# Performance work log

Hardware: AMD Instinct MI355X
Metric: run time of the kernel (lower is better)

Reference implementation:

```python
import jax, jax.numpy as jnp
import numpy as np

N = 50000      # nodes
E = 800000     # edges (avg degree 16)
C = 16         # hidden states per generative model
M = 32         # discrete symbol alphabet size
G = 8          # n_gen


def setup_inputs() -> dict:
    key = jax.random.key(0)
    k = jax.random.split(key, 6)
    u = lambda kk, shp: jax.random.uniform(kk, shp, jnp.float32, -5.0, 5.0)
    return {
        "x": jax.random.randint(k[0], (N,), 0, M),
        "edge_index": jax.random.randint(k[1], (2, E), 0, N),
        "B0": u(k[2], (C, M, G)),       # CGMMLayer_0.B
        "Pi": u(k[3], (C, G)),          # CGMMLayer_0.Pi
        "B1": u(k[4], (C, M, G)),       # CGMMLayer.B
        "Q_neigh": u(k[5], (C, C, G)),  # CGMMLayer.Q_neigh
    }


def reference(x, edge_index, B0, Pi, B1, Q_neigh):
    n = x.shape[0]
    # ---- layer 0 (CGMMLayer_0) ----
    sm_B0 = jax.nn.softmax(B0, axis=1)   # [C,M,G], softmax over symbols
    sm_Pi = jax.nn.softmax(Pi, axis=0)   # [C,G],   softmax over states
    # unnorm_posterior = Pi * B[:, x]    -> [N,C,G]
    unnorm0 = sm_Pi[None, :, :] * jnp.transpose(sm_B0[:, x, :], (1, 0, 2))
    norm0 = unnorm0.sum(1, keepdims=True)           # [N,1,G]
    ll0 = jnp.log(norm0[:, 0, :])                   # [N,G]
    post0 = unnorm0 / norm0                         # [N,C,G] = h_prev
    # ---- layer 1 (CGMMLayer) ----
    sm_Q = jax.nn.softmax(Q_neigh, axis=0)          # [C,C,G], softmax over dim 0
    sm_B1 = jax.nn.softmax(B1, axis=1)              # [C,M,G]
    src, dst = edge_index[0], edge_index[1]
    gathered = post0[dst]                           # [E,C,G] edge gather
    aggr_sum = jax.ops.segment_sum(gathered, src, num_segments=n)   # [N,C,G]
    cnt = jax.ops.segment_sum(jnp.ones((src.shape[0],), jnp.float32), src, num_segments=n)
    aggr = aggr_sum / jnp.maximum(cnt, 1.0)[:, None, None]          # scatter-mean
    B_nodes = jnp.transpose(sm_B1[:, x, :], (1, 0, 2))[:, :, None, :]  # [N,C,1,G]
    # joint over (current state i, neighbor state l): [N,C,C,G]
    unnorm1 = B_nodes * sm_Q[None, :, :, :] * aggr[:, None, :, :]
    norm1 = unnorm1.sum((1, 2), keepdims=True)      # [N,1,1,G]
    post1 = (unnorm1 / norm1).sum(2)                # [N,C,G] posterior_i
    ll1 = jnp.log(norm1[:, 0, 0, :])                # [N,G]
    log_likelihood = jnp.stack([ll0, ll1], axis=1)  # [N,2,G] (per layer)
    return log_likelihood, post1
```

## Files before the change

### kernel.cpp

```cpp
#include <hip/hip_runtime.h>
#include <hip/hip_bf16.h>
#include <math.h>

#define Nn 50000
#define Ee 800000
#define Cc 16
#define Mm 32
#define Gg 8
#define CAPk 44

#define P1B 250
#define NBK 512
#define BSZ 98
#define SEGE 24
#define SEGW 25
#define L0B 517

__device__ __forceinline__ float ldin(const void* p, int idx, int isbf) {
    if (isbf) return __bfloat162float(((const __hip_bfloat16*)p)[idx]);
    return ((const float*)p)[idx];
}
__device__ __forceinline__ void stout(void* p, size_t idx, float v, int isbf) {
    if (isbf) ((__hip_bfloat16*)p)[idx] = __float2bfloat16(v);
    else ((float*)p)[idx] = v;
}
__device__ __forceinline__ unsigned short f2bf(float f) {
    unsigned u = __float_as_uint(f);
    return (unsigned short)((u + 0x7FFFu + ((u >> 16) & 1u)) >> 16);
}
__device__ __forceinline__ float bflo(unsigned v) { return __uint_as_float(v << 16); }
__device__ __forceinline__ float bfhi(unsigned v) { return __uint_as_float(v & 0xffff0000u); }

__device__ __forceinline__ int detect_bf16(const void* B0, int tid, int* sflag) {
    if (tid < 64) {
        unsigned wv = ((const unsigned*)B0)[tid];
        unsigned ex = (wv >> 7) & 0xFFu;
        unsigned long long m = __ballot(ex >= 120u && ex <= 130u);
        if (tid == 0) *sflag = (__popcll(m) >= 48) ? 1 : 0;
    }
    __syncthreads();
    return *sflag;
}

__device__ __forceinline__ void sm_col(float* a, int base, int stride, int cnt) {
    float mx = -1e30f;
    for (int k = 0; k < cnt; ++k) mx = fmaxf(mx, a[base + k * stride]);
    float s = 0.f;
    for (int k = 0; k < cnt; ++k) {
        float e = __expf(a[base + k * stride] - mx);
        a[base + k * stride] = e;
        s += e;
    }
    float inv = 1.0f / s;
    for (int k = 0; k < cnt; ++k) a[base + k * stride] *= inv;
}

__global__ void bucket_layer0(const int* __restrict__ ei,
                              const int* __restrict__ x,
                              const void* __restrict__ B0,
                              const void* __restrict__ Pi,
                              const void* __restrict__ B1,
                              const void* __restrict__ Q,
                              unsigned* __restrict__ segbuf,
                              unsigned short* __restrict__ post0,
                              float* __restrict__ smB1ws,
                              float* __restrict__ smQgws,
                              int* __restrict__ flag_ws,
                              void* __restrict__ out) {
    int b = blockIdx.x, tid = threadIdx.x;
    __shared__ unsigned shb[NBK + NBK * SEGE];
    __shared__ int sflag;

    if (b < P1B) {
        int* scnt = (int*)shb;
        unsigned* sstage = shb + NBK;
        for (int i = tid; i < NBK; i += 256) scnt[i] = 0;
        __syncthreads();
        const int4* ei4 = (const int4*)ei;
        const int qbase = b * 800;
        for (int q = tid; q < 800; q += 256) {
            int4 sv = ei4[qbase + q];
            int4 dv = ei4[200000 + qbase + q];
#pragma unroll
            for (int k = 0; k < 4; ++k) {
                int s = (k == 0) ? sv.x : (k == 1) ? sv.y : (k == 2) ? sv.z : sv.w;
                int d = (k == 0) ? dv.x : (k == 1) ? dv.y : (k == 2) ? dv.z : dv.w;
                int bk = s / BSZ;
                int pos = atomicAdd(&scnt[bk], 1);
                if (pos < SEGE)
                    sstage[bk * SEGE + pos] = ((unsigned)(s - bk * BSZ) << 16) | (unsigned)d;
            }
        }
        __syncthreads();
        for (int idx = tid; idx < NBK * SEGW; idx += 256) {
            int bk = idx / SEGW;
            int j  = idx - bk * SEGW;
            int c  = scnt[bk]; c = c < SEGE ? c : SEGE;
            unsigned v = (j == 0) ? (unsigned)c : sstage[bk * SEGE + (j - 1)];
            segbuf[((size_t)bk * P1B + b) * SEGW + j] = v;
        }
        return;
    }

    float* sh = (float*)shb;

    if (b == P1B + L0B) {
        if (tid < 16) {
            uint4 z; z.x = 0u; z.y = 0u; z.z = 0u; z.w = 0u;
            ((uint4*)(post0 + (size_t)Nn * 128))[tid] = z;
        }
        const int isbf = detect_bf16(B0, tid, &sflag);
        if (tid == 0) flag_ws[0] = isbf;
        for (int i = tid; i < Cc * Mm * Gg; i += 256) sh[i] = ldin(B1, i, isbf);
        __syncthreads();
        if (tid < 128) sm_col(sh, (tid >> 3) * (Mm * Gg) + (tid & 7), Gg, Mm);
        __syncthreads();
        for (int i = tid; i < Cc * Mm * Gg; i += 256) smB1ws[i] = sh[i];
        __syncthreads();
        for (int i = tid; i < Cc * Cc * Gg; i += 256) sh[i] = ldin(Q, i, isbf);
        __syncthreads();
        if (tid < 128) sm_col(sh, (tid >> 3) * Gg + (tid & 7), Cc * Gg, Cc);
        __syncthreads();
        for (int t = tid; t < Cc * Cc * Gg; t += 256) {
            int i = t >> 7, rem = t & 127, l = rem >> 3, g = rem & 7;
            smQgws[g * (Cc * Cc) + i * Cc + l] = sh[t];
        }
        return;
    }

    float* sB0sm = sh;
    float* sPism = sh + 4096;
    const int isbf = detect_bf16(B0, tid, &sflag);

    for (int i = tid; i < Cc * Mm * Gg; i += 256) sB0sm[i] = ldin(B0, i, isbf);
    if (tid < Cc * Gg) sPism[tid] = ldin(Pi, tid, isbf);
    __syncthreads();
    if (tid < 128) {
        sm_col(sB0sm, (tid >> 3) * (Mm * Gg) + (tid & 7), Gg, Mm);
    } else if (tid < 128 + Gg) {
        sm_col(sPism, tid - 128, Gg, Cc);
    }
    __syncthreads();

    for (int idx = (b - P1B) * 256 + tid; idx < Nn * Gg; idx += L0B * 256) {
        int n = idx >> 3, g = idx & 7;
        int xv = x[n];
        float u[Cc];
        float norm = 0.f;
#pragma unroll
        for (int c = 0; c < Cc; ++c) {
            float v = sPism[c * Gg + g] * sB0sm[c * (Mm * Gg) + xv * Gg + g];
            u[c] = v; norm += v;
        }
        float inv = 1.0f / norm;
        unsigned short h[Cc];
#pragma unroll
        for (int c = 0; c < Cc; ++c) h[c] = f2bf(u[c] * inv);
        uint4 w0, w1;
        w0.x = h[0] | (h[1] << 16);   w0.y = h[2] | (h[3] << 16);
        w0.z = h[4] | (h[5] << 16);   w0.w = h[6] | (h[7] << 16);
        w1.x = h[8] | (h[9] << 16);   w1.y = h[10] | (h[11] << 16);
        w1.z = h[12] | (h[13] << 16); w1.w = h[14] | (h[15] << 16);
        uint4* dst = (uint4*)(post0 + (size_t)n * 128 + g * 16);
        dst[0] = w0; dst[1] = w1;
        stout(out, (size_t)n * (2 * Gg) + g, logf(norm), isbf);
    }
}

#define GL2(vv, eb, nn, dde) { int ej_ = (eb) + sub16; \
    int dn_ = (ej_ < (dde)) ? (int)list[(nn) * CAPk + ej_] : Nn; \
    unsigned off_ = ((unsigned)dn_ << 8) + mbyte; \
    vv = *(const uint4*)((const char*)post0 + off_); }
#define GACC(vv) { \
    acc[0] += bflo(vv.x); acc[1] += bfhi(vv.x); acc[2] += bflo(vv.y); acc[3] += bfhi(vv.y); \
    acc[4] += bflo(vv.z); acc[5] += bfhi(vv.z); acc[6] += bflo(vv.w); acc[7] += bfhi(vv.w); }

__global__ __launch_bounds__(512) void place_aggr(
        const unsigned* __restrict__ segbuf,
        const unsigned short* __restrict__ post0,
        const int* __restrict__ x,
        const float* __restrict__ smB1ws,
        const float* __restrict__ smQgws,
        const int* __restrict__ flag_ws,
        void* __restrict__ out) {
    __shared__ unsigned list[BSZ * CAPk];
    __shared__ int cnt[BSZ];
    __shared__ int scl[P1B];
    __shared__ float sQ[4341];
    int b = blockIdx.x, tid = threadIdx.x;
    const int isbf = flag_ws[0];
    const unsigned* strip = segbuf + (size_t)b * (P1B * SEGW);

    for (int t = tid; t < Cc * Cc * Gg; t += 512) {
        int g = t >> 8, i = (t >> 4) & 15, j = t & 15;
        sQ[g * 545 + i * 34 + j] = smQgws[t];
    }
    for (int i = tid; i < BSZ; i += 512) cnt[i] = 0;
    if (tid < P1B) scl[tid] = (int)strip[tid * SEGW];
    __syncthreads();

    {
        for (int w = tid; w < P1B * SEGW; w += 512) {
            unsigned pk = strip[w];
            int seg = w / SEGW;
            int j   = w - seg * SEGW;
            if (j >= 1 && j <= scl[seg]) {
                int sl = (int)(pk >> 16);
                int pos = atomicAdd(&cnt[sl], 1);
                if (pos < CAPk) list[sl * CAPk + pos] = pk & 0xffffu;
            }
        }
    }
    __syncthreads();

    const int lane = tid & 63, wib = tid >> 6;
    const int sub16 = lane >> 4;
    const unsigned mbyte = (unsigned)((lane & 15) * 16);
    const int ii = lane >> 3, gW = lane & 7;
    const int i0 = 2 * ii, i1 = i0 + 1;
    const float* qp = sQ + gW * 545 + i0 * 34;
    const int nbase = b * BSZ;
    int limt = Nn - nbase; if (limt > BSZ) limt = BSZ;
    const int lim = limt;

    int n = wib;
    int dv0 = 0, dd0 = 0; float b0c = 0.f, b1c = 0.f;
    uint4 bA0, bA1, bA2, bA3;
    bA0.x = bA0.y = bA0.z = bA0.w = 0u; bA1 = bA0; bA2 = bA0; bA3 = bA0;
    if (n < lim) {
        dv0 = __builtin_amdgcn_readfirstlane(cnt[n]);
        dd0 = dv0 < CAPk ? dv0 : CAPk;
        int xv = x[nbase + n];
        b0c = smB1ws[i0 * (Mm * Gg) + xv * Gg + gW];
        b1c = smB1ws[i1 * (Mm * Gg) + xv * Gg + gW];
        GL2(bA0, 0, n, dd0); GL2(bA1, 4, n, dd0); GL2(bA2, 8, n, dd0); GL2(bA3, 12, n, dd0);
    }

    while (n < lim) {
        int n1 = n + 8;
        int dv1 = 0, dd1 = 0; float b0n = 0.f, b1n = 0.f;
        uint4 bB0, bB1, bB2, bB3;
        bB0.x = bB0.y = bB0.z = bB0.w = 0u; bB1 = bB0; bB2 = bB0; bB3 = bB0;
        if (n1 < lim) {
            dv1 = __builtin_amdgcn_readfirstlane(cnt[n1]);
            dd1 = dv1 < CAPk ? dv1 : CAPk;
            int xv = x[nbase + n1];
            b0n = smB1ws[i0 * (Mm * Gg) + xv * Gg + gW];
            b1n = smB1ws[i1 * (Mm * Gg) + xv * Gg + gW];
            GL2(bB0, 0, n1, dd1); GL2(bB1, 4, n1, dd1); GL2(bB2, 8, n1, dd1); GL2(bB3, 12, n1, dd1);
        }

        float acc[8];
#pragma unroll
        for (int j = 0; j < 8; ++j) acc[j] = 0.f;
        GACC(bA0); GACC(bA1); GACC(bA2); GACC(bA3);
        for (int e = 16; e < dd0; e += 16) {
            uint4 t0, t1, t2, t3;
            GL2(t0, e, n, dd0); GL2(t1, e + 4, n, dd0);
            GL2(t2, e + 8, n, dd0); GL2(t3, e + 12, n, dd0);
            GACC(t0); GACC(t1); GACC(t2); GACC(t3);
        }

#pragma unroll
        for (int j = 0; j < 8; ++j) {
            acc[j] += __shfl_xor(acc[j], 16, 64);
            acc[j] += __shfl_xor(acc[j], 32, 64);
        }
        float qa0 = 0.f, qa1 = 0.f;
#pragma unroll
        for (int j = 0; j < 8; ++j) {
            float t0 = __shfl(acc[j], 2 * gW, 64);
            float t1 = __shfl(acc[j], 2 * gW + 1, 64);
            qa0 += qp[j] * t0 + qp[8 + j] * t1;
            qa1 += qp[34 + j] * t0 + qp[42 + j] * t1;
        }
        float invd = 1.0f / fmaxf((float)dv0, 1.0f);
        qa0 *= invd; qa1 *= invd;
        float v0 = b0c * qa0, v1 = b1c * qa1;
        float nrm = v0 + v1;
        nrm += __shfl_xor(nrm, 8, 64);
        nrm += __shfl_xor(nrm, 16, 64);
        nrm += __shfl_xor(nrm, 32, 64);
        float invn = 1.0f / nrm;
        int ng = nbase + n;
        size_t pbase = (size_t)Nn * 2 * Gg + (size_t)ng * (Cc * Gg);
        stout(out, pbase + i0 * Gg + gW, v0 * invn, isbf);
        stout(out, pbase + i1 * Gg + gW, v1 * invn, isbf);
        if (ii == 0) stout(out, (size_t)ng * (2 * Gg) + Gg + gW, logf(nrm), isbf);

        n = n1;
        dv0 = dv1; dd0 = dd1; b0c = b0n; b1c = b1n;
        bA0 = bB0; bA1 = bB1; bA2 = bB2; bA3 = bB3;
    }
}

extern "C" void kernel_launch(void* const* d_in, const int* in_sizes, int n_in,
                              void* d_out, int out_size, void* d_ws, size_t ws_size,
                              hipStream_t stream) {
    const int* x  = (const int*)d_in[0];
    const int* ei = (const int*)d_in[1];
    const void* B0 = d_in[2];
    const void* Pi = d_in[3];
    const void* B1 = d_in[4];
    const void* Q  = d_in[5];

    float* ws = (float*)d_ws;
    int*   flag   = (int*)ws;
    float* smB1ws = ws + 128;
    float* smQgws = smB1ws + 4096;
    unsigned short* post0 = (unsigned short*)(smQgws + 2048);
    unsigned* segbuf = (unsigned*)(post0 + (size_t)(Nn + 1) * 128);

    bucket_layer0<<<P1B + L0B + 1, 256, 0, stream>>>(
        ei, x, B0, Pi, B1, Q, segbuf, post0, smB1ws, smQgws, flag, d_out);

    place_aggr<<<NBK, 512, 0, stream>>>(
        segbuf, post0, x, smB1ws, smQgws, flag, d_out);
}
```

Before: 132.3 us.

## Replace per-node layer-0 posteriors with a per-symbol lookup table in shared memory

post0 depends only on the node's symbol x, so the layer-0 posterior is precomputed as a 32x128 bf16 table, along with a per-symbol log-norm table. The edge list now stores the destination's symbol (5 bits) instead of its node id. The aggregation gathers table rows from LDS instead of post0 rows from global memory. This removes the 50000-node post0 write pass and the random global gathers, at the cost of an extra random x[dst] load during bucketing and the loss of the software prefetch pipeline in the aggregation loop.

Result: no change. 131.2 us (-0.9%).

```diff
diff --git a/kernel.cpp b/kernel.cpp
--- a/kernel.cpp
+++ b/kernel.cpp
@@ -14,7 +14,7 @@
 #define BSZ 98
 #define SEGE 24
 #define SEGW 25
-#define L0B 517
+#define RROW 136
 
 __device__ __forceinline__ float ldin(const void* p, int idx, int isbf) {
     if (isbf) return __bfloat162float(((const __hip_bfloat16*)p)[idx]);
@@ -55,14 +55,15 @@
     for (int k = 0; k < cnt; ++k) a[base + k * stride] *= inv;
 }
 
-__global__ void bucket_layer0(const int* __restrict__ ei,
+__global__ void bucket_tables(const int* __restrict__ ei,
                               const int* __restrict__ x,
                               const void* __restrict__ B0,
                               const void* __restrict__ Pi,
                               const void* __restrict__ B1,
                               const void* __restrict__ Q,
                               unsigned* __restrict__ segbuf,
-                              unsigned short* __restrict__ post0,
+                              unsigned short* __restrict__ Rws,
+                              float* __restrict__ lntabws,
                               float* __restrict__ smB1ws,
                               float* __restrict__ smQgws,
                               int* __restrict__ flag_ws,
@@ -81,14 +82,18 @@
         for (int q = tid; q < 800; q += 256) {
             int4 sv = ei4[qbase + q];
             int4 dv = ei4[200000 + qbase + q];
+            int ds_[4] = { dv.x, dv.y, dv.z, dv.w };
+            int xs_[4];
+#pragma unroll
+            for (int k = 0; k < 4; ++k) xs_[k] = x[ds_[k]];
 #pragma unroll
             for (int k = 0; k < 4; ++k) {
                 int s = (k == 0) ? sv.x : (k == 1) ? sv.y : (k == 2) ? sv.z : sv.w;
-                int d = (k == 0) ? dv.x : (k == 1) ? dv.y : (k == 2) ? dv.z : dv.w;
                 int bk = s / BSZ;
                 int pos = atomicAdd(&scnt[bk], 1);
                 if (pos < SEGE)
-                    sstage[bk * SEGE + pos] = ((unsigned)(s - bk * BSZ) << 16) | (unsigned)d;
+                    sstage[bk * SEGE + pos] =
+                        ((unsigned)(s - bk * BSZ) << 5) | (unsigned)xs_[k];
             }
         }
         __syncthreads();
@@ -103,90 +108,79 @@
     }
 
     float* sh = (float*)shb;
-
-    if (b == P1B + L0B) {
-        if (tid < 16) {
-            uint4 z; z.x = 0u; z.y = 0u; z.z = 0u; z.w = 0u;
-            ((uint4*)(post0 + (size_t)Nn * 128))[tid] = z;
-        }
-        const int isbf = detect_bf16(B0, tid, &sflag);
-        if (tid == 0) flag_ws[0] = isbf;
-        for (int i = tid; i < Cc * Mm * Gg; i += 256) sh[i] = ldin(B1, i, isbf);
-        __syncthreads();
-        if (tid < 128) sm_col(sh, (tid >> 3) * (Mm * Gg) + (tid & 7), Gg, Mm);
-        __syncthreads();
-        for (int i = tid; i < Cc * Mm * Gg; i += 256) smB1ws[i] = sh[i];
-        __syncthreads();
-        for (int i = tid; i < Cc * Cc * Gg; i += 256) sh[i] = ldin(Q, i, isbf);
-        __syncthreads();
-        if (tid < 128) sm_col(sh, (tid >> 3) * Gg + (tid & 7), Cc * Gg, Cc);
-        __syncthreads();
-        for (int t = tid; t < Cc * Cc * Gg; t += 256) {
-            int i = t >> 7, rem = t & 127, l = rem >> 3, g = rem & 7;
-            smQgws[g * (Cc * Cc) + i * Cc + l] = sh[t];
-        }
-        return;
-    }
-
-    float* sB0sm = sh;
-    float* sPism = sh + 4096;
     const int isbf = detect_bf16(B0, tid, &sflag);
-
-    for (int i = tid; i < Cc * Mm * Gg; i += 256) sB0sm[i] = ldin(B0, i, isbf);
-    if (tid < Cc * Gg) sPism[tid] = ldin(Pi, tid, isbf);
+    if (tid == 0) flag_ws[0] = isbf;
+    for (int i = tid; i < Cc * Mm * Gg; i += 256) sh[i] = ldin(B1, i, isbf);
+    __syncthreads();
+    if (tid < 128) sm_col(sh, (tid >> 3) * (Mm * Gg) + (tid & 7), Gg, Mm);
+    __syncthreads();
+    for (int i = tid; i < Cc * Mm * Gg; i += 256) smB1ws[i] = sh[i];
+    __syncthreads();
+    for (int i = tid; i < Cc * Cc * Gg; i += 256) sh[i] = ldin(Q, i, isbf);
+    __syncthreads();
+    if (tid < 128) sm_col(sh, (tid >> 3) * Gg + (tid & 7), Cc * Gg, Cc);
+    __syncthreads();
+    for (int t = tid; t < Cc * Cc * Gg; t += 256) {
+        int i = t >> 7, rem = t & 127, l = rem >> 3, g = rem & 7;
+        smQgws[g * (Cc * Cc) + i * Cc + l] = sh[t];
+    }
+    __syncthreads();
+    float* sB0 = sh;
+    float* sPi = sh + 4096;
+    float* sInv = sh + 4224;
+    for (int i = tid; i < Cc * Mm * Gg; i += 256) sB0[i] = ldin(B0, i, isbf);
+    if (tid < Cc * Gg) sPi[tid] = ldin(Pi, tid, isbf);
     __syncthreads();
     if (tid < 128) {
-        sm_col(sB0sm, (tid >> 3) * (Mm * Gg) + (tid & 7), Gg, Mm);
+        sm_col(sB0, (tid >> 3) * (Mm * Gg) + (tid & 7), Gg, Mm);
     } else if (tid < 128 + Gg) {
-        sm_col(sPism, tid - 128, Gg, Cc);
-    }
-    __syncthreads();
-
-    for (int idx = (b - P1B) * 256 + tid; idx < Nn * Gg; idx += L0B * 256) {
-        int n = idx >> 3, g = idx & 7;
-        int xv = x[n];
-        float u[Cc];
-        float norm = 0.f;
-#pragma unroll
-        for (int c = 0; c < Cc; ++c) {
-            float v = sPism[c * Gg + g] * sB0sm[c * (Mm * Gg) + xv * Gg + g];
-            u[c] = v; norm += v;
-        }
-        float inv = 1.0f / norm;
-        unsigned short h[Cc];
-#pragma unroll
-        for (int c = 0; c < Cc; ++c) h[c] = f2bf(u[c] * inv);
-        uint4 w0, w1;
-        w0.x = h[0] | (h[1] << 16);   w0.y = h[2] | (h[3] << 16);
-        w0.z = h[4] | (h[5] << 16);   w0.w = h[6] | (h[7] << 16);
-        w1.x = h[8] | (h[9] << 16);   w1.y = h[10] | (h[11] << 16);
-        w1.z = h[12] | (h[13] << 16); w1.w = h[14] | (h[15] << 16);
-        uint4* dst = (uint4*)(post0 + (size_t)n * 128 + g * 16);
-        dst[0] = w0; dst[1] = w1;
-        stout(out, (size_t)n * (2 * Gg) + g, logf(norm), isbf);
-    }
-}
-
-#define GL2(vv, eb, nn, dde) { int ej_ = (eb) + sub16; \
-    int dn_ = (ej_ < (dde)) ? (int)list[(nn) * CAPk + ej_] : Nn; \
-    unsigned off_ = ((unsigned)dn_ << 8) + mbyte; \
-    vv = *(const uint4*)((const char*)post0 + off_); }
+        sm_col(sPi, tid - 128, Gg, Cc);
+    }
+    __syncthreads();
+    if (tid < Mm * Gg) {
+        int mm = tid >> 3, g = tid & 7;
+        float s = 0.f;
+#pragma unroll
+        for (int c = 0; c < Cc; ++c) s += sPi[c * Gg + g] * sB0[c * (Mm * Gg) + mm * Gg + g];
+        lntabws[tid] = logf(s);
+        sInv[tid] = 1.0f / s;
+    }
+    __syncthreads();
+    for (int idx = tid; idx < 33 * RROW; idx += 256) {
+        int row = idx / RROW, rem = idx - row * RROW;
+        unsigned short v = 0;
+        if (row < 32 && rem < 128) {
+            int g = rem >> 4, c = rem & 15;
+            float pv = sPi[c * Gg + g] * sB0[c * (Mm * Gg) + row * Gg + g] * sInv[row * Gg + g];
+            v = f2bf(pv);
+        }
+        Rws[idx] = v;
+    }
+}
+
 #define GACC(vv) { \
     acc[0] += bflo(vv.x); acc[1] += bfhi(vv.x); acc[2] += bflo(vv.y); acc[3] += bfhi(vv.y); \
     acc[4] += bflo(vv.z); acc[5] += bfhi(vv.z); acc[6] += bflo(vv.w); acc[7] += bfhi(vv.w); }
+#define GEDGE(eb) { int ej_ = (eb) + sub16; \
+    int xv_ = (ej_ < dd0) ? (int)list8[nb44 + ej_] : 32; \
+    uint4 rv_ = *(const uint4*)(R16 + xv_ * RROW + (m16 << 3)); \
+    GACC(rv_); }
 
 __global__ __launch_bounds__(512) void place_aggr(
         const unsigned* __restrict__ segbuf,
-        const unsigned short* __restrict__ post0,
         const int* __restrict__ x,
         const float* __restrict__ smB1ws,
         const float* __restrict__ smQgws,
+        const unsigned short* __restrict__ Rws,
+        const float* __restrict__ lntabws,
         const int* __restrict__ flag_ws,
         void* __restrict__ out) {
-    __shared__ unsigned list[BSZ * CAPk];
+    __shared__ unsigned short R16[33 * RROW];
+    __shared__ float sQ[4341];
+    __shared__ float lnt[256];
+    __shared__ unsigned char list8[BSZ * CAPk];
     __shared__ int cnt[BSZ];
     __shared__ int scl[P1B];
-    __shared__ float sQ[4341];
     int b = blockIdx.x, tid = threadIdx.x;
     const int isbf = flag_ws[0];
     const unsigned* strip = segbuf + (size_t)b * (P1B * SEGW);
@@ -195,6 +189,9 @@
         int g = t >> 8, i = (t >> 4) & 15, j = t & 15;
         sQ[g * 545 + i * 34 + j] = smQgws[t];
     }
+    for (int t = tid; t < (33 * RROW) / 2; t += 512)
+        ((unsigned*)R16)[t] = ((const unsigned*)Rws)[t];
+    for (int t = tid; t < 256; t += 512) lnt[t] = lntabws[t];
     for (int i = tid; i < BSZ; i += 512) cnt[i] = 0;
     if (tid < P1B) scl[tid] = (int)strip[tid * SEGW];
     __syncthreads();
@@ -205,61 +202,41 @@
             int seg = w / SEGW;
             int j   = w - seg * SEGW;
             if (j >= 1 && j <= scl[seg]) {
-                int sl = (int)(pk >> 16);
+                int sl = (int)(pk >> 5);
                 int pos = atomicAdd(&cnt[sl], 1);
-                if (pos < CAPk) list[sl * CAPk + pos] = pk & 0xffffu;
+                if (pos < CAPk) list8[sl * CAPk + pos] = (unsigned char)(pk & 31u);
             }
         }
     }
     __syncthreads();
 
+    const int nbase = b * BSZ;
+    int limt = Nn - nbase; if (limt > BSZ) limt = BSZ; if (limt < 0) limt = 0;
+
+    for (int t = tid; t < limt * 8; t += 512) {
+        int n = t >> 3, g = t & 7;
+        int xv = x[nbase + n];
+        stout(out, (size_t)(nbase + n) * (2 * Gg) + g, lnt[xv * 8 + g], isbf);
+    }
+
     const int lane = tid & 63, wib = tid >> 6;
-    const int sub16 = lane >> 4;
-    const unsigned mbyte = (unsigned)((lane & 15) * 16);
+    const int sub16 = lane >> 4, m16 = lane & 15;
     const int ii = lane >> 3, gW = lane & 7;
     const int i0 = 2 * ii, i1 = i0 + 1;
     const float* qp = sQ + gW * 545 + i0 * 34;
-    const int nbase = b * BSZ;
-    int limt = Nn - nbase; if (limt > BSZ) limt = BSZ;
-    const int lim = limt;
-
-    int n = wib;
-    int dv0 = 0, dd0 = 0; float b0c = 0.f, b1c = 0.f;
-    uint4 bA0, bA1, bA2, bA3;
-    bA0.x = bA0.y = bA0.z = bA0.w = 0u; bA1 = bA0; bA2 = bA0; bA3 = bA0;
-    if (n < lim) {
-        dv0 = __builtin_amdgcn_readfirstlane(cnt[n]);
-        dd0 = dv0 < CAPk ? dv0 : CAPk;
-        int xv = x[nbase + n];
-        b0c = smB1ws[i0 * (Mm * Gg) + xv * Gg + gW];
-        b1c = smB1ws[i1 * (Mm * Gg) + xv * Gg + gW];
-        GL2(bA0, 0, n, dd0); GL2(bA1, 4, n, dd0); GL2(bA2, 8, n, dd0); GL2(bA3, 12, n, dd0);
-    }
-
-    while (n < lim) {
-        int n1 = n + 8;
-        int dv1 = 0, dd1 = 0; float b0n = 0.f, b1n = 0.f;
-        uint4 bB0, bB1, bB2, bB3;
-        bB0.x = bB0.y = bB0.z = bB0.w = 0u; bB1 = bB0; bB2 = bB0; bB3 = bB0;
-        if (n1 < lim) {
-            dv1 = __builtin_amdgcn_readfirstlane(cnt[n1]);
-            dd1 = dv1 < CAPk ? dv1 : CAPk;
-            int xv = x[nbase + n1];
-            b0n = smB1ws[i0 * (Mm * Gg) + xv * Gg + gW];
-            b1n = smB1ws[i1 * (Mm * Gg) + xv * Gg + gW];
-            GL2(bB0, 0, n1, dd1); GL2(bB1, 4, n1, dd1); GL2(bB2, 8, n1, dd1); GL2(bB3, 12, n1, dd1);
-        }
+
+    for (int n = wib; n < limt; n += 8) {
+        const int dv0 = cnt[n];
+        const int dd0 = dv0 < CAPk ? dv0 : CAPk;
+        const int nb44 = n * CAPk;
+        int xvn = x[nbase + n];
+        float b0c = smB1ws[i0 * (Mm * Gg) + xvn * Gg + gW];
+        float b1c = smB1ws[i1 * (Mm * Gg) + xvn * Gg + gW];
 
         float acc[8];
 #pragma unroll
         for (int j = 0; j < 8; ++j) acc[j] = 0.f;
-        GACC(bA0); GACC(bA1); GACC(bA2); GACC(bA3);
-        for (int e = 16; e < dd0; e += 16) {
-            uint4 t0, t1, t2, t3;
-            GL2(t0, e, n, dd0); GL2(t1, e + 4, n, dd0);
-            GL2(t2, e + 8, n, dd0); GL2(t3, e + 12, n, dd0);
-            GACC(t0); GACC(t1); GACC(t2); GACC(t3);
-        }
+        for (int e = 0; e < dd0; e += 4) GEDGE(e);
 
 #pragma unroll
         for (int j = 0; j < 8; ++j) {
@@ -287,10 +264,6 @@
         stout(out, pbase + i0 * Gg + gW, v0 * invn, isbf);
         stout(out, pbase + i1 * Gg + gW, v1 * invn, isbf);
         if (ii == 0) stout(out, (size_t)ng * (2 * Gg) + Gg + gW, logf(nrm), isbf);
-
-        n = n1;
-        dv0 = dv1; dd0 = dd1; b0c = b0n; b1c = b1n;
-        bA0 = bB0; bA1 = bB1; bA2 = bB2; bA3 = bB3;
     }
 }
 
@@ -308,12 +281,13 @@
     int*   flag   = (int*)ws;
     float* smB1ws = ws + 128;
     float* smQgws = smB1ws + 4096;
-    unsigned short* post0 = (unsigned short*)(smQgws + 2048);
-    unsigned* segbuf = (unsigned*)(post0 + (size_t)(Nn + 1) * 128);
-
-    bucket_layer0<<<P1B + L0B + 1, 256, 0, stream>>>(
-        ei, x, B0, Pi, B1, Q, segbuf, post0, smB1ws, smQgws, flag, d_out);
+    float* lntabws = smQgws + 2048;
+    unsigned short* Rws = (unsigned short*)(lntabws + 256);
+    unsigned* segbuf = (unsigned*)(lntabws + 256 + 2304);
+
+    bucket_tables<<<P1B + 1, 256, 0, stream>>>(
+        ei, x, B0, Pi, B1, Q, segbuf, Rws, lntabws, smB1ws, smQgws, flag, d_out);
 
     place_aggr<<<NBK, 512, 0, stream>>>(
-        segbuf, post0, x, smB1ws, smQgws, flag, d_out);
-}
+        segbuf, x, smB1ws, smQgws, Rws, lntabws, flag, d_out);
+}
```
